# Kernel tuning notes

Measured on AMD Instinct MI355X. Metric: run time of the kernel, lower is better.

The kernel has to match this reference:

```python
import jax, jax.numpy as jnp
import numpy as np

B, S, D = 4, 2048, 1024


def setup_inputs() -> dict:
    key = jax.random.key(0)
    ks = jax.random.split(key, 11)
    sc = 0.02
    f32 = jnp.float32
    return {
        "x1": jax.random.normal(ks[0], (B, S, D), f32),
        "x2": jax.random.normal(ks[1], (B, S, D), f32),
        "x3": jax.random.normal(ks[2], (B, S, D), f32),
        # Stacked per-modality projection weights, stored (in, out) so y = x @ W + b
        "Wq": jax.random.normal(ks[3], (3, D, D), f32) * sc,
        "bq": jax.random.normal(ks[4], (3, D), f32) * sc,
        "Wk": jax.random.normal(ks[5], (3, D, D), f32) * sc,
        "bk": jax.random.normal(ks[6], (3, D), f32) * sc,
        "Wv": jax.random.normal(ks[7], (3, D, D), f32) * sc,
        "bv": jax.random.normal(ks[8], (3, D), f32) * sc,
        "Wo": jax.random.normal(ks[9], (3, 2 * D, D), f32) * sc,
        "bo": jax.random.normal(ks[10], (3, D), f32) * sc,
    }


def reference(x1, x2, x3, Wq, bq, Wk, bk, Wv, bv, Wo, bo):
    x = jnp.stack([x1, x2, x3])                      # (3, B, S, D)
    q = jnp.einsum('mbsd,mde->mbse', x, Wq) + bq[:, None, None, :]
    k = jnp.einsum('mbsd,mde->mbse', x, Wk) + bk[:, None, None, :]
    v = jnp.einsum('mbsd,mde->mbse', x, Wv) + bv[:, None, None, :]
    scale = 1.0 / jnp.sqrt(jnp.asarray(x.shape[-1], x.dtype))
    # self-scores per modality: q_i @ k_i^T
    scores = jnp.einsum('mbsd,mbtd->mbst', q, k) * scale   # (3, B, S, S)
    attn = jax.nn.softmax(scores, axis=-1)
    # context_i = attn_i @ v_{(i+1) mod 3}  (1->2, 2->3, 3->1); dropout is eval-mode identity
    v_next = jnp.roll(v, shift=-1, axis=0)
    ctx = jnp.einsum('mbst,mbtd->mbsd', attn, v_next)      # (3, B, S, D)
    comb = jnp.concatenate([x, ctx], axis=-1)              # (3, B, S, 2D)
    out = jnp.einsum('mbsf,mfd->mbsd', comb, Wo) + bo[:, None, None, :]
    global_feature = jnp.concatenate([out[0], out[1], out[2]], axis=1)  # (B, 3S, D)
    return out[0], out[1], out[2], global_feature
```

## Files before the change

kernel.cpp:

```cpp
#include <hip/hip_runtime.h>
#include <hip/hip_bf16.h>

typedef __bf16 bf16_t;
typedef __bf16 bf16x8 __attribute__((ext_vector_type(8)));
typedef float f32x4 __attribute__((ext_vector_type(4)));

typedef __attribute__((address_space(1))) unsigned int as1_uint;
typedef __attribute__((address_space(3))) unsigned int as3_uint;

#define Bsz 4
#define Ssz 2048
#define Dsz 1024
#define BSD (Bsz * Ssz * Dsz)
#define SCALE_ 0.03125f

__device__ __forceinline__ void gll16(const void* g, void* l) {
  __builtin_amdgcn_global_load_lds((const as1_uint*)g, (as3_uint*)l, 16, 0, 0);
}

__device__ __forceinline__ unsigned bfbits(float f) {
  union { bf16_t h; unsigned short u; } c;
  c.h = (bf16_t)f;
  return (unsigned)c.u;
}

__device__ __forceinline__ void gemm_core(char* AsB, char* BsB,
                                          const bf16_t* A, const bf16_t* A2, int ksplit,
                                          int lda, int lda2,
                                          const bf16_t* Bt, int ldb,
                                          int ktiles, f32x4 acc[4][4]) {
  const int tid = threadIdx.x;
  const int wave = tid >> 6, lane = tid & 63;
  const int quad = lane >> 4, m16 = lane & 15, x7 = lane & 7;
  const int waveM = (wave >> 1) << 6, waveN = (wave & 1) << 6;
  const int srow = tid >> 3;
  const int schunk = (tid & 7) ^ ((tid >> 3) & 7);
  const int ldsbase = wave << 10;

  for (int kt = 0; kt < ktiles; ++kt) {
    const bf16_t* Ak = (kt < ksplit) ? (A + kt * 64) : (A2 + (kt - ksplit) * 64);
    const int ldak = (kt < ksplit) ? lda : lda2;
    const bf16_t* Bk = Bt + kt * 64;
    __syncthreads();
#pragma unroll
    for (int it = 0; it < 4; ++it)
      gll16(Ak + (size_t)(it * 32 + srow) * ldak + schunk * 8, AsB + it * 4096 + ldsbase);
#pragma unroll
    for (int it = 0; it < 4; ++it)
      gll16(Bk + (size_t)(it * 32 + srow) * ldb + schunk * 8, BsB + it * 4096 + ldsbase);
    __syncthreads();
#pragma unroll
    for (int t = 0; t < 2; ++t) {
      bf16x8 a[4], b[4];
      const int cc = t * 4 + quad;
#pragma unroll
      for (int i = 0; i < 4; ++i) {
        const int rr = waveM + i * 16 + m16;
        a[i] = *(const bf16x8*)(AsB + rr * 128 + ((cc ^ x7) << 4));
      }
#pragma unroll
      for (int j = 0; j < 4; ++j) {
        const int rr = waveN + j * 16 + m16;
        b[j] = *(const bf16x8*)(BsB + rr * 128 + ((cc ^ x7) << 4));
      }
#pragma unroll
      for (int i = 0; i < 4; ++i)
#pragma unroll
        for (int j = 0; j < 4; ++j)
          acc[i][j] = __builtin_amdgcn_mfma_f32_16x16x32_bf16(b[j], a[i], acc[i][j], 0, 0, 0);
    }
  }
}

__device__ __forceinline__ ushort4 pack4(const f32x4 v, const float4 b) {
  ushort4 u;
  u.x = (unsigned short)bfbits(v[0] + b.x);
  u.y = (unsigned short)bfbits(v[1] + b.y);
  u.z = (unsigned short)bfbits(v[2] + b.z);
  u.w = (unsigned short)bfbits(v[3] + b.w);
  return u;
}

__global__ __launch_bounds__(256, 2)
void gemm_bt_bf16(const bf16_t* __restrict__ A, long long sAz, int lda,
                  const bf16_t* __restrict__ Bt, long long sBz, int ldb,
                  bf16_t* __restrict__ C, long long sCz, int ldc,
                  int K, int rollB) {
  __shared__ __attribute__((aligned(16))) char smem[32768];
  const int z = blockIdx.z;
  int zb = z;
  if (rollB) { const int m = z >> 2, b = z & 3; zb = ((m + 1) % 3) * Bsz + b; }
  const bf16_t* Az = A + (long long)z * sAz + (size_t)blockIdx.y * 128 * lda;
  const bf16_t* Bz = Bt + (long long)zb * sBz + (size_t)blockIdx.x * 128 * ldb;
  f32x4 acc[4][4];
  const f32x4 zero = {0.f, 0.f, 0.f, 0.f};
#pragma unroll
  for (int i = 0; i < 4; ++i)
#pragma unroll
    for (int j = 0; j < 4; ++j) acc[i][j] = zero;

  gemm_core(smem, smem + 16384, Az, Az, 1 << 30, lda, lda, Bz, ldb, K / 64, acc);

  const int lane = threadIdx.x & 63, wave = threadIdx.x >> 6;
  const int Mb = blockIdx.y * 128 + ((wave >> 1) << 6) + (lane & 15);
  const int Nb = blockIdx.x * 128 + ((wave & 1) << 6) + ((lane >> 4) << 2);
  bf16_t* Cz = C + (long long)z * sCz;
  const float4 zb4 = {0.f, 0.f, 0.f, 0.f};
#pragma unroll
  for (int i = 0; i < 4; ++i) {
    const int M = Mb + i * 16;
#pragma unroll
    for (int j = 0; j < 4; ++j) {
      const int N = Nb + j * 16;
      *(ushort4*)(Cz + (size_t)M * ldc + N) = pack4(acc[i][j], zb4);
    }
  }
}

__global__ __launch_bounds__(256, 2)
void gemm_qkv(const bf16_t* __restrict__ xb, const bf16_t* __restrict__ Wqkvt,
              const float* __restrict__ bq, const float* __restrict__ bk,
              const float* __restrict__ bvp,
              bf16_t* __restrict__ Q, bf16_t* __restrict__ Kb, bf16_t* __restrict__ Vt) {
  __shared__ __attribute__((aligned(16))) char smem[34048];
  const int m = blockIdx.z;
  const int x = blockIdx.x;
  const int which = x >> 3;
  const bf16_t* Az = xb + (size_t)m * BSD + (size_t)blockIdx.y * 128 * Dsz;
  const bf16_t* Bz = Wqkvt + (size_t)m * 3145728 + (size_t)x * 131072;
  f32x4 acc[4][4];
  const f32x4 zero = {0.f, 0.f, 0.f, 0.f};
#pragma unroll
  for (int i = 0; i < 4; ++i)
#pragma unroll
    for (int j = 0; j < 4; ++j) acc[i][j] = zero;

  gemm_core(smem, smem + 16384, Az, Az, 1 << 30, Dsz, Dsz, Bz, Dsz, 16, acc);

  const int tid = threadIdx.x;
  const int lane = tid & 63, wave = tid >> 6;
  const int Ml = ((wave >> 1) << 6) + (lane & 15);
  const int Nl = ((wave & 1) << 6) + ((lane >> 4) << 2);
  const int dseg0 = (x & 7) * 128;
  const float* bb = (which == 0 ? bq : which == 1 ? bk : bvp) + m * Dsz;

  if (which < 2) {
    bf16_t* Cz = (which == 0 ? Q : Kb) + (size_t)m * BSD;
#pragma unroll
    for (int j = 0; j < 4; ++j) {
      const int N = Nl + j * 16;
      const float4 b4 = *(const float4*)(bb + dseg0 + N);
#pragma unroll
      for (int i = 0; i < 4; ++i) {
        const int M = blockIdx.y * 128 + Ml + i * 16;
        *(ushort4*)(Cz + (size_t)M * Dsz + dseg0 + N) = pack4(acc[i][j], b4);
      }
    }
  } else {
    unsigned short* T = (unsigned short*)smem;
    __syncthreads();
#pragma unroll
    for (int j = 0; j < 4; ++j) {
      const int N = Nl + j * 16;
      const float4 b4 = *(const float4*)(bb + dseg0 + N);
      const float bia[4] = {b4.x, b4.y, b4.z, b4.w};
#pragma unroll
      for (int i = 0; i < 4; ++i) {
        const int M = Ml + i * 16;
#pragma unroll
        for (int r = 0; r < 4; ++r)
          T[(N + r) * 132 + M] = (unsigned short)bfbits(acc[i][j][r] + bia[r]);
      }
    }
    __syncthreads();
    const int b = blockIdx.y >> 4;
    const int s0 = (blockIdx.y & 15) * 128;
    bf16_t* Vz = Vt + ((size_t)(m * 4 + b) * 1024 + dseg0) * Ssz;
#pragma unroll
    for (int e = 0; e < 16; ++e) {
      const int idx = e * 256 + tid;
      const int nl = idx >> 5, mc = (idx & 31) * 4;
      const ushort4 u = *(const ushort4*)(T + nl * 132 + mc);
      *(ushort4*)(Vz + (size_t)nl * Ssz + s0 + mc) = u;
    }
  }
}

__global__ __launch_bounds__(256, 2)
void gemm_out(const bf16_t* __restrict__ xb, const bf16_t* __restrict__ ctx,
              const bf16_t* __restrict__ Wot, const float* __restrict__ bo,
              float* __restrict__ out) {
  __shared__ __attribute__((aligned(16))) char smem[32768];
  const int m = blockIdx.z;
  const bf16_t* Az = xb + (size_t)m * BSD + (size_t)blockIdx.y * 128 * Dsz;
  const bf16_t* A2z = ctx + (size_t)m * BSD + (size_t)blockIdx.y * 128 * Dsz;
  const bf16_t* Bz = Wot + (size_t)m * (Dsz * 2 * Dsz) + (size_t)blockIdx.x * 128 * (2 * Dsz);
  f32x4 acc[4][4];
  const f32x4 zero = {0.f, 0.f, 0.f, 0.f};
#pragma unroll
  for (int i = 0; i < 4; ++i)
#pragma unroll
    for (int j = 0; j < 4; ++j) acc[i][j] = zero;

  gemm_core(smem, smem + 16384, Az, A2z, 16, Dsz, Dsz, Bz, 2 * Dsz, 32, acc);

  const int lane = threadIdx.x & 63, wave = threadIdx.x >> 6;
  const int Mb = blockIdx.y * 128 + ((wave >> 1) << 6) + (lane & 15);
  const int Nb = blockIdx.x * 128 + ((wave & 1) << 6) + ((lane >> 4) << 2);
  const float* bz = bo + m * Dsz;
#pragma unroll
  for (int i = 0; i < 4; ++i) {
    const int M = Mb + i * 16;
    const int b = M >> 11, s = M & 2047;
    float* o1 = out + (size_t)m * BSD + (size_t)M * Dsz;
    float* o2 = out + (size_t)3 * BSD + (size_t)b * (3 * Ssz * Dsz) + (size_t)(m * Ssz + s) * Dsz;
#pragma unroll
    for (int j = 0; j < 4; ++j) {
      const int N = Nb + j * 16;
      const float4 b4 = *(const float4*)(bz + N);
      float4 o;
      o.x = acc[i][j][0] + b4.x; o.y = acc[i][j][1] + b4.y;
      o.z = acc[i][j][2] + b4.z; o.w = acc[i][j][3] + b4.w;
      *(float4*)(o1 + N) = o;
      *(float4*)(o2 + N) = o;
    }
  }
}

__global__ __launch_bounds__(256)
void cvt_x(const float* __restrict__ x1, const float* __restrict__ x2,
           const float* __restrict__ x3, bf16_t* __restrict__ xb) {
  const size_t i = ((size_t)blockIdx.x * 256 + threadIdx.x) * 4;
  const float* src;
  size_t off;
  if (i < (size_t)BSD)          { src = x1; off = i; }
  else if (i < (size_t)2 * BSD) { src = x2; off = i - BSD; }
  else                          { src = x3; off = i - (size_t)2 * BSD; }
  const float4 v = *(const float4*)(src + off);
  union { bf16_t h[4]; uint2 u; } o;
  o.h[0] = (bf16_t)v.x; o.h[1] = (bf16_t)v.y; o.h[2] = (bf16_t)v.z; o.h[3] = (bf16_t)v.w;
  *(uint2*)(xb + i) = o.u;
}

__global__ __launch_bounds__(256)
void transpose_to_bf16(const float* __restrict__ in, bf16_t* __restrict__ out,
                       int ldin, int ldout, long long sIn, long long sOut) {
  __shared__ bf16_t Ts[64][65];
  const int t = threadIdx.x;
  const long long z = blockIdx.z;
  const float* inz = in + z * sIn;
  bf16_t* outz = out + z * sOut;
  const int r0 = blockIdx.y << 6, c0 = blockIdx.x << 6;
#pragma unroll
  for (int e = 0; e < 4; ++e) {
    const int idx = (e * 256 + t) * 4;
    const int rr = idx >> 6, cc = idx & 63;
    const float4 v = *(const float4*)(inz + (size_t)(r0 + rr) * ldin + (c0 + cc));
    Ts[rr][cc] = (bf16_t)v.x; Ts[rr][cc + 1] = (bf16_t)v.y;
    Ts[rr][cc + 2] = (bf16_t)v.z; Ts[rr][cc + 3] = (bf16_t)v.w;
  }
  __syncthreads();
#pragma unroll
  for (int e = 0; e < 4; ++e) {
    const int idx = (e * 256 + t) * 4;
    const int oc = idx >> 6, orr = idx & 63;
    union { bf16_t h[4]; uint2 u; } o4;
    o4.h[0] = Ts[orr][oc]; o4.h[1] = Ts[orr + 1][oc];
    o4.h[2] = Ts[orr + 2][oc]; o4.h[3] = Ts[orr + 3][oc];
    *(uint2*)(outz + (size_t)(c0 + oc) * ldout + (r0 + orr)) = o4.u;
  }
}

__global__ __launch_bounds__(256)
void softmax_rows(bf16_t* __restrict__ Sc) {
  const size_t row = blockIdx.x;
  uint4* p = (uint4*)(Sc + row * Ssz);
  const int t = threadIdx.x;
  const int lane = t & 63, wave = t >> 6;
  uint4 u = p[t];
  float v[8];
  v[0] = __uint_as_float(u.x << 16); v[1] = __uint_as_float(u.x & 0xffff0000u);
  v[2] = __uint_as_float(u.y << 16); v[3] = __uint_as_float(u.y & 0xffff0000u);
  v[4] = __uint_as_float(u.z << 16); v[5] = __uint_as_float(u.z & 0xffff0000u);
  v[6] = __uint_as_float(u.w << 16); v[7] = __uint_as_float(u.w & 0xffff0000u);

  float mx = v[0];
#pragma unroll
  for (int i = 1; i < 8; ++i) mx = fmaxf(mx, v[i]);
  for (int o = 32; o > 0; o >>= 1) mx = fmaxf(mx, __shfl_xor(mx, o));
  __shared__ float redm[4], reds[4];
  if (lane == 0) redm[wave] = mx;
  __syncthreads();
  mx = fmaxf(fmaxf(redm[0], redm[1]), fmaxf(redm[2], redm[3]));

  float s = 0.f;
#pragma unroll
  for (int i = 0; i < 8; ++i) { v[i] = __expf((v[i] - mx) * SCALE_); s += v[i]; }
  for (int o = 32; o > 0; o >>= 1) s += __shfl_xor(s, o);
  if (lane == 0) reds[wave] = s;
  __syncthreads();
  s = reds[0] + reds[1] + reds[2] + reds[3];
  const float inv = 1.0f / s;
#pragma unroll
  for (int i = 0; i < 8; ++i) v[i] *= inv;

  u.x = bfbits(v[0]) | (bfbits(v[1]) << 16);
  u.y = bfbits(v[2]) | (bfbits(v[3]) << 16);
  u.z = bfbits(v[4]) | (bfbits(v[5]) << 16);
  u.w = bfbits(v[6]) | (bfbits(v[7]) << 16);
  p[t] = u;
}

extern "C" void kernel_launch(void* const* d_in, const int* in_sizes, int n_in,
                              void* d_out, int out_size, void* d_ws, size_t ws_size,
                              hipStream_t stream) {
  const float* x1 = (const float*)d_in[0];
  const float* x2 = (const float*)d_in[1];
  const float* x3 = (const float*)d_in[2];
  const float* Wq = (const float*)d_in[3];
  const float* bq = (const float*)d_in[4];
  const float* Wk = (const float*)d_in[5];
  const float* bk = (const float*)d_in[6];
  const float* Wv = (const float*)d_in[7];
  const float* bv = (const float*)d_in[8];
  const float* Wo = (const float*)d_in[9];
  const float* bo = (const float*)d_in[10];

  char* ws = (char*)d_ws;
  bf16_t* xb    = (bf16_t*)(ws + 0);
  bf16_t* Wqkvt = (bf16_t*)(ws + 50331648);
  bf16_t* Wot   = (bf16_t*)(ws + 69206016);
  bf16_t* Q     = (bf16_t*)(ws + 81788928);
  bf16_t* Kb    = (bf16_t*)(ws + 132120576);
  bf16_t* Vt    = (bf16_t*)(ws + 182452224);
  bf16_t* Sc    = (bf16_t*)d_out;
  bf16_t* ctx   = Q;

  cvt_x<<<24576, 256, 0, stream>>>(x1, x2, x3, xb);
  transpose_to_bf16<<<dim3(16, 16, 3), 256, 0, stream>>>(Wq, Wqkvt + 0,       1024, 1024, 1048576LL, 3145728LL);
  transpose_to_bf16<<<dim3(16, 16, 3), 256, 0, stream>>>(Wk, Wqkvt + 1048576, 1024, 1024, 1048576LL, 3145728LL);
  transpose_to_bf16<<<dim3(16, 16, 3), 256, 0, stream>>>(Wv, Wqkvt + 2097152, 1024, 1024, 1048576LL, 3145728LL);
  transpose_to_bf16<<<dim3(16, 32, 3), 256, 0, stream>>>(Wo, Wot, 1024, 2048, 2097152LL, 2097152LL);
  gemm_qkv<<<dim3(24, 64, 3), 256, 0, stream>>>(xb, Wqkvt, bq, bk, bv, Q, Kb, Vt);
  gemm_bt_bf16<<<dim3(16, 16, 12), 256, 0, stream>>>(Q, 2097152LL, Dsz, Kb, 2097152LL, Dsz, Sc, 4194304LL, Ssz, Dsz, 0);
  softmax_rows<<<24576, 256, 0, stream>>>(Sc);
  gemm_bt_bf16<<<dim3(8, 16, 12), 256, 0, stream>>>(Sc, 4194304LL, Ssz, Vt, 2097152LL, Ssz, ctx, 2097152LL, Dsz, Ssz, 1);
  gemm_out<<<dim3(8, 64, 3), 256, 0, stream>>>(xb, ctx, Wot, bo, (float*)d_out);
}
```

Measured before the change: 901.1 us.

## Replace GEMM core with 256x256 double-buffered, phase-interleaved 8-wave pipeline

Replaces the 128x128 single-buffered GEMM core with a 256x256 tile, 512-thread core. It double-buffers K tiles in 128KB of LDS, issues global-to-LDS loads for tile t+2 interleaved with MFMA phases, and raises MFMA priority with setprio. All four GEMM kernels, their epilogues (including the V transpose, now done in two halves) and the launch grids are updated to match. The aim is to hide load latency and improve data reuse per byte loaded. The cost is much higher LDS and register pressure per block, so occupancy will be lower, and the grids are smaller.

```diff
diff --git a/kernel.cpp b/kernel.cpp
--- a/kernel.cpp
+++ b/kernel.cpp
@@ -22,54 +22,6 @@
   union { bf16_t h; unsigned short u; } c;
   c.h = (bf16_t)f;
   return (unsigned)c.u;
-}
-
-__device__ __forceinline__ void gemm_core(char* AsB, char* BsB,
-                                          const bf16_t* A, const bf16_t* A2, int ksplit,
-                                          int lda, int lda2,
-                                          const bf16_t* Bt, int ldb,
-                                          int ktiles, f32x4 acc[4][4]) {
-  const int tid = threadIdx.x;
-  const int wave = tid >> 6, lane = tid & 63;
-  const int quad = lane >> 4, m16 = lane & 15, x7 = lane & 7;
-  const int waveM = (wave >> 1) << 6, waveN = (wave & 1) << 6;
-  const int srow = tid >> 3;
-  const int schunk = (tid & 7) ^ ((tid >> 3) & 7);
-  const int ldsbase = wave << 10;
-
-  for (int kt = 0; kt < ktiles; ++kt) {
-    const bf16_t* Ak = (kt < ksplit) ? (A + kt * 64) : (A2 + (kt - ksplit) * 64);
-    const int ldak = (kt < ksplit) ? lda : lda2;
-    const bf16_t* Bk = Bt + kt * 64;
-    __syncthreads();
-#pragma unroll
-    for (int it = 0; it < 4; ++it)
-      gll16(Ak + (size_t)(it * 32 + srow) * ldak + schunk * 8, AsB + it * 4096 + ldsbase);
-#pragma unroll
-    for (int it = 0; it < 4; ++it)
-      gll16(Bk + (size_t)(it * 32 + srow) * ldb + schunk * 8, BsB + it * 4096 + ldsbase);
-    __syncthreads();
-#pragma unroll
-    for (int t = 0; t < 2; ++t) {
-      bf16x8 a[4], b[4];
-      const int cc = t * 4 + quad;
-#pragma unroll
-      for (int i = 0; i < 4; ++i) {
-        const int rr = waveM + i * 16 + m16;
-        a[i] = *(const bf16x8*)(AsB + rr * 128 + ((cc ^ x7) << 4));
-      }
-#pragma unroll
-      for (int j = 0; j < 4; ++j) {
-        const int rr = waveN + j * 16 + m16;
-        b[j] = *(const bf16x8*)(BsB + rr * 128 + ((cc ^ x7) << 4));
-      }
-#pragma unroll
-      for (int i = 0; i < 4; ++i)
-#pragma unroll
-        for (int j = 0; j < 4; ++j)
-          acc[i][j] = __builtin_amdgcn_mfma_f32_16x16x32_bf16(b[j], a[i], acc[i][j], 0, 0, 0);
-    }
-  }
 }
 
 __device__ __forceinline__ ushort4 pack4(const f32x4 v, const float4 b) {
@@ -81,146 +33,272 @@
   return u;
 }
 
-__global__ __launch_bounds__(256, 2)
+__device__ __forceinline__ void mf8(f32x4 acc[8][4], int ib, int jb,
+                                    const bf16x8 b[2], const bf16x8 a[4]) {
+  __builtin_amdgcn_s_setprio(1);
+#pragma unroll
+  for (int i = 0; i < 4; ++i)
+#pragma unroll
+    for (int j = 0; j < 2; ++j)
+      acc[ib + i][jb + j] = __builtin_amdgcn_mfma_f32_16x16x32_bf16(
+          b[j], a[i], acc[ib + i][jb + j], 0, 0, 0);
+  __builtin_amdgcn_s_setprio(0);
+}
+
+#define PHASE_BAR() do {                                   \
+    asm volatile("s_waitcnt lgkmcnt(0)" ::: "memory");     \
+    __builtin_amdgcn_sched_barrier(0);                     \
+    __builtin_amdgcn_s_barrier();                          \
+    __builtin_amdgcn_sched_barrier(0);                     \
+  } while (0)
+
+__device__ __forceinline__ void gemm_core256(char* smem,
+    const bf16_t* A, const bf16_t* A2, int ks, int lda,
+    const bf16_t* Bt, int ldb, int KT, f32x4 acc[8][4]) {
+  const int tid = threadIdx.x;
+  const int wave = tid >> 6, lane = tid & 63;
+  const int quad = lane >> 4, m16 = lane & 15;
+  const int wm = wave >> 2, wn = wave & 3;
+  const int swz = ((quad ^ ((m16 >> 1) & 3)) << 4);
+  const int Ab = ((wm * 128 + m16) << 6) + swz;
+  const int Bb = 32768 + ((wn * 64 + m16) << 6) + swz;
+
+  const int srow = tid >> 2;
+  const int sg = (((tid & 3) ^ ((srow >> 1) & 3)) << 3);
+  const size_t aoff = (size_t)srow * lda + sg;
+  const size_t boff = (size_t)srow * ldb + sg;
+  const size_t astep = (size_t)128 * lda;
+  const size_t bstep = (size_t)128 * ldb;
+  char* ldsW = smem + (wave << 10);
+
+  auto stageA = [&](const bf16_t* As, int sb, int kh) {
+    const bf16_t* s = As + aoff + kh * 32;
+    char* d = ldsW + sb + kh * 16384;
+    gll16(s, d);
+    gll16(s + astep, d + 8192);
+  };
+  auto stageB = [&](const bf16_t* Bs, int sb, int kh) {
+    const bf16_t* s = Bs + boff + kh * 32;
+    char* d = ldsW + sb + 32768 + kh * 16384;
+    gll16(s, d);
+    gll16(s + bstep, d + 8192);
+  };
+
+#pragma unroll
+  for (int t0 = 0; t0 < 2; ++t0) {
+    const bf16_t* As = (t0 < ks) ? (A + t0 * 64) : (A2 + (t0 - ks) * 64);
+    const bf16_t* Bs = Bt + t0 * 64;
+    const int sb = t0 << 16;
+    stageB(Bs, sb, 0); stageB(Bs, sb, 1);
+    stageA(As, sb, 0); stageA(As, sb, 1);
+  }
+
+  bf16x8 a0[4], a1[4], b00[2], b01[2], b10[2], b11[2];
+
+#pragma unroll 1
+  for (int t = 0; t < KT; ++t) {
+    const int cur = (t & 1) << 16;
+    const int tp = (t + 2 < KT) ? (t + 2) : (KT - 1);
+    const bf16_t* As = (tp < ks) ? (A + tp * 64) : (A2 + (tp - ks) * 64);
+    const bf16_t* Bs = Bt + tp * 64;
+    const char* sbp = smem + cur;
+
+    asm volatile("s_waitcnt vmcnt(8)" ::: "memory");
+    __builtin_amdgcn_sched_barrier(0);
+    __builtin_amdgcn_s_barrier();
+    __builtin_amdgcn_sched_barrier(0);
+
+#pragma unroll
+    for (int i = 0; i < 4; ++i) a0[i] = *(const bf16x8*)(sbp + (Ab + i * 1024));
+#pragma unroll
+    for (int j = 0; j < 2; ++j) b00[j] = *(const bf16x8*)(sbp + (Bb + j * 1024));
+    mf8(acc, 0, 0, b00, a0);
+
+#pragma unroll
+    for (int i = 0; i < 4; ++i) a1[i] = *(const bf16x8*)(sbp + (16384 + Ab + i * 1024));
+#pragma unroll
+    for (int j = 0; j < 2; ++j) b01[j] = *(const bf16x8*)(sbp + (16384 + Bb + j * 1024));
+    mf8(acc, 0, 0, b01, a1);
+
+#pragma unroll
+    for (int j = 0; j < 2; ++j) b10[j] = *(const bf16x8*)(sbp + (Bb + 2048 + j * 1024));
+    mf8(acc, 0, 2, b10, a0);
+    PHASE_BAR();
+
+    stageB(Bs, cur, 0);
+#pragma unroll
+    for (int j = 0; j < 2; ++j) b11[j] = *(const bf16x8*)(sbp + (16384 + Bb + 2048 + j * 1024));
+    mf8(acc, 0, 2, b11, a1);
+    PHASE_BAR();
+
+    stageB(Bs, cur, 1);
+#pragma unroll
+    for (int i = 0; i < 4; ++i) a0[i] = *(const bf16x8*)(sbp + (Ab + 4096 + i * 1024));
+    mf8(acc, 4, 0, b00, a0);
+    PHASE_BAR();
+
+    stageA(As, cur, 0);
+#pragma unroll
+    for (int i = 0; i < 4; ++i) a1[i] = *(const bf16x8*)(sbp + (16384 + Ab + 4096 + i * 1024));
+    mf8(acc, 4, 0, b01, a1);
+    PHASE_BAR();
+
+    stageA(As, cur, 1);
+    mf8(acc, 4, 2, b10, a0);
+
+    mf8(acc, 4, 2, b11, a1);
+  }
+
+  asm volatile("s_waitcnt vmcnt(0)" ::: "memory");
+  __builtin_amdgcn_sched_barrier(0);
+}
+
+#define EPI_VARS                                               \
+  const int tid = threadIdx.x, lane = tid & 63, wave = tid >> 6; \
+  const int quad = lane >> 4, m16 = lane & 15;                 \
+  const int wm = wave >> 2, wn = wave & 3;                     \
+  (void)tid; (void)quad; (void)m16; (void)wm; (void)wn;
+#define MLOC(ip) (wm * 128 + (((ip) >> 2) << 6) + (((ip) & 3) << 4) + m16)
+#define NLOC(jp) (wn * 64 + (((jp) >> 1) << 5) + (((jp) & 1) << 4) + (quad << 2))
+
+__global__ __launch_bounds__(512, 2)
 void gemm_bt_bf16(const bf16_t* __restrict__ A, long long sAz, int lda,
                   const bf16_t* __restrict__ Bt, long long sBz, int ldb,
                   bf16_t* __restrict__ C, long long sCz, int ldc,
                   int K, int rollB) {
-  __shared__ __attribute__((aligned(16))) char smem[32768];
+  __shared__ __attribute__((aligned(16))) char smem[131072];
   const int z = blockIdx.z;
   int zb = z;
   if (rollB) { const int m = z >> 2, b = z & 3; zb = ((m + 1) % 3) * Bsz + b; }
-  const bf16_t* Az = A + (long long)z * sAz + (size_t)blockIdx.y * 128 * lda;
-  const bf16_t* Bz = Bt + (long long)zb * sBz + (size_t)blockIdx.x * 128 * ldb;
-  f32x4 acc[4][4];
+  const bf16_t* Az = A + (long long)z * sAz + (size_t)blockIdx.y * 256 * lda;
+  const bf16_t* Bz = Bt + (long long)zb * sBz + (size_t)blockIdx.x * 256 * ldb;
+  f32x4 acc[8][4];
   const f32x4 zero = {0.f, 0.f, 0.f, 0.f};
 #pragma unroll
-  for (int i = 0; i < 4; ++i)
+  for (int i = 0; i < 8; ++i)
 #pragma unroll
     for (int j = 0; j < 4; ++j) acc[i][j] = zero;
 
-  gemm_core(smem, smem + 16384, Az, Az, 1 << 30, lda, lda, Bz, ldb, K / 64, acc);
-
-  const int lane = threadIdx.x & 63, wave = threadIdx.x >> 6;
-  const int Mb = blockIdx.y * 128 + ((wave >> 1) << 6) + (lane & 15);
-  const int Nb = blockIdx.x * 128 + ((wave & 1) << 6) + ((lane >> 4) << 2);
+  gemm_core256(smem, Az, Az, 1 << 30, lda, Bz, ldb, K / 64, acc);
+
+  EPI_VARS;
   bf16_t* Cz = C + (long long)z * sCz;
   const float4 zb4 = {0.f, 0.f, 0.f, 0.f};
 #pragma unroll
-  for (int i = 0; i < 4; ++i) {
-    const int M = Mb + i * 16;
-#pragma unroll
-    for (int j = 0; j < 4; ++j) {
-      const int N = Nb + j * 16;
-      *(ushort4*)(Cz + (size_t)M * ldc + N) = pack4(acc[i][j], zb4);
+  for (int ip = 0; ip < 8; ++ip) {
+    const size_t M = (size_t)blockIdx.y * 256 + MLOC(ip);
+#pragma unroll
+    for (int jp = 0; jp < 4; ++jp) {
+      const int N = blockIdx.x * 256 + NLOC(jp);
+      *(ushort4*)(Cz + M * ldc + N) = pack4(acc[ip][jp], zb4);
     }
   }
 }
 
-__global__ __launch_bounds__(256, 2)
+__global__ __launch_bounds__(512, 2)
 void gemm_qkv(const bf16_t* __restrict__ xb, const bf16_t* __restrict__ Wqkvt,
               const float* __restrict__ bq, const float* __restrict__ bk,
               const float* __restrict__ bvp,
               bf16_t* __restrict__ Q, bf16_t* __restrict__ Kb, bf16_t* __restrict__ Vt) {
-  __shared__ __attribute__((aligned(16))) char smem[34048];
+  __shared__ __attribute__((aligned(16))) char smem[131072];
   const int m = blockIdx.z;
   const int x = blockIdx.x;
-  const int which = x >> 3;
-  const bf16_t* Az = xb + (size_t)m * BSD + (size_t)blockIdx.y * 128 * Dsz;
-  const bf16_t* Bz = Wqkvt + (size_t)m * 3145728 + (size_t)x * 131072;
-  f32x4 acc[4][4];
+  const int which = x >> 2;
+  const bf16_t* Az = xb + (size_t)m * BSD + (size_t)blockIdx.y * 256 * Dsz;
+  const bf16_t* Bz = Wqkvt + (size_t)m * 3145728 + (size_t)x * 262144;
+  f32x4 acc[8][4];
   const f32x4 zero = {0.f, 0.f, 0.f, 0.f};
 #pragma unroll
-  for (int i = 0; i < 4; ++i)
+  for (int i = 0; i < 8; ++i)
 #pragma unroll
     for (int j = 0; j < 4; ++j) acc[i][j] = zero;
 
-  gemm_core(smem, smem + 16384, Az, Az, 1 << 30, Dsz, Dsz, Bz, Dsz, 16, acc);
-
-  const int tid = threadIdx.x;
-  const int lane = tid & 63, wave = tid >> 6;
-  const int Ml = ((wave >> 1) << 6) + (lane & 15);
-  const int Nl = ((wave & 1) << 6) + ((lane >> 4) << 2);
-  const int dseg0 = (x & 7) * 128;
+  gemm_core256(smem, Az, Az, 1 << 30, Dsz, Bz, Dsz, 16, acc);
+
+  EPI_VARS;
+  const int dseg0 = (x & 3) * 256;
   const float* bb = (which == 0 ? bq : which == 1 ? bk : bvp) + m * Dsz;
 
   if (which < 2) {
     bf16_t* Cz = (which == 0 ? Q : Kb) + (size_t)m * BSD;
 #pragma unroll
-    for (int j = 0; j < 4; ++j) {
-      const int N = Nl + j * 16;
+    for (int jp = 0; jp < 4; ++jp) {
+      const int N = NLOC(jp);
       const float4 b4 = *(const float4*)(bb + dseg0 + N);
 #pragma unroll
-      for (int i = 0; i < 4; ++i) {
-        const int M = blockIdx.y * 128 + Ml + i * 16;
-        *(ushort4*)(Cz + (size_t)M * Dsz + dseg0 + N) = pack4(acc[i][j], b4);
+      for (int ip = 0; ip < 8; ++ip) {
+        const size_t M = (size_t)blockIdx.y * 256 + MLOC(ip);
+        *(ushort4*)(Cz + M * Dsz + dseg0 + N) = pack4(acc[ip][jp], b4);
       }
     }
   } else {
     unsigned short* T = (unsigned short*)smem;
-    __syncthreads();
-#pragma unroll
-    for (int j = 0; j < 4; ++j) {
-      const int N = Nl + j * 16;
-      const float4 b4 = *(const float4*)(bb + dseg0 + N);
-      const float bia[4] = {b4.x, b4.y, b4.z, b4.w};
-#pragma unroll
-      for (int i = 0; i < 4; ++i) {
-        const int M = Ml + i * 16;
-#pragma unroll
-        for (int r = 0; r < 4; ++r)
-          T[(N + r) * 132 + M] = (unsigned short)bfbits(acc[i][j][r] + bia[r]);
+    const int b = blockIdx.y >> 3;
+    const int s0 = (blockIdx.y & 7) * 256;
+    bf16_t* Vz = Vt + ((size_t)(m * 4 + b) * 1024 + dseg0) * (size_t)Ssz;
+#pragma unroll
+    for (int nh = 0; nh < 2; ++nh) {
+      __syncthreads();
+      if ((wn >> 1) == nh) {
+#pragma unroll
+        for (int jp = 0; jp < 4; ++jp) {
+          const int Nh = ((wn & 1) << 6) + (((jp) >> 1) << 5) + (((jp) & 1) << 4) + (quad << 2);
+          const float4 b4 = *(const float4*)(bb + dseg0 + nh * 128 + Nh);
+          const float bia[4] = {b4.x, b4.y, b4.z, b4.w};
+#pragma unroll
+          for (int ip = 0; ip < 8; ++ip) {
+            const int M = MLOC(ip);
+#pragma unroll
+            for (int r = 0; r < 4; ++r)
+              T[(Nh + r) * 264 + M] = (unsigned short)bfbits(acc[ip][jp][r] + bia[r]);
+          }
+        }
+      }
+      __syncthreads();
+#pragma unroll
+      for (int e = 0; e < 8; ++e) {
+        const int c = e * 512 + tid;
+        const int n = c >> 5, mc = (c & 31) * 8;
+        *(uint4*)(Vz + (size_t)(nh * 128 + n) * Ssz + s0 + mc) =
+            *(const uint4*)(T + n * 264 + mc);
       }
     }
-    __syncthreads();
-    const int b = blockIdx.y >> 4;
-    const int s0 = (blockIdx.y & 15) * 128;
-    bf16_t* Vz = Vt + ((size_t)(m * 4 + b) * 1024 + dseg0) * Ssz;
-#pragma unroll
-    for (int e = 0; e < 16; ++e) {
-      const int idx = e * 256 + tid;
-      const int nl = idx >> 5, mc = (idx & 31) * 4;
-      const ushort4 u = *(const ushort4*)(T + nl * 132 + mc);
-      *(ushort4*)(Vz + (size_t)nl * Ssz + s0 + mc) = u;
-    }
-  }
-}
-
-__global__ __launch_bounds__(256, 2)
+  }
+}
+
+__global__ __launch_bounds__(512, 2)
 void gemm_out(const bf16_t* __restrict__ xb, const bf16_t* __restrict__ ctx,
               const bf16_t* __restrict__ Wot, const float* __restrict__ bo,
               float* __restrict__ out) {
-  __shared__ __attribute__((aligned(16))) char smem[32768];
+  __shared__ __attribute__((aligned(16))) char smem[131072];
   const int m = blockIdx.z;
-  const bf16_t* Az = xb + (size_t)m * BSD + (size_t)blockIdx.y * 128 * Dsz;
-  const bf16_t* A2z = ctx + (size_t)m * BSD + (size_t)blockIdx.y * 128 * Dsz;
-  const bf16_t* Bz = Wot + (size_t)m * (Dsz * 2 * Dsz) + (size_t)blockIdx.x * 128 * (2 * Dsz);
-  f32x4 acc[4][4];
+  const bf16_t* Az = xb + (size_t)m * BSD + (size_t)blockIdx.y * 256 * Dsz;
+  const bf16_t* A2z = ctx + (size_t)m * BSD + (size_t)blockIdx.y * 256 * Dsz;
+  const bf16_t* Bz = Wot + (size_t)m * (Dsz * 2 * Dsz) + (size_t)blockIdx.x * 256 * (2 * Dsz);
+  f32x4 acc[8][4];
   const f32x4 zero = {0.f, 0.f, 0.f, 0.f};
 #pragma unroll
-  for (int i = 0; i < 4; ++i)
+  for (int i = 0; i < 8; ++i)
 #pragma unroll
     for (int j = 0; j < 4; ++j) acc[i][j] = zero;
 
-  gemm_core(smem, smem + 16384, Az, A2z, 16, Dsz, Dsz, Bz, 2 * Dsz, 32, acc);
-
-  const int lane = threadIdx.x & 63, wave = threadIdx.x >> 6;
-  const int Mb = blockIdx.y * 128 + ((wave >> 1) << 6) + (lane & 15);
-  const int Nb = blockIdx.x * 128 + ((wave & 1) << 6) + ((lane >> 4) << 2);
+  gemm_core256(smem, Az, A2z, 16, Dsz, Bz, 2 * Dsz, 32, acc);
+
+  EPI_VARS;
   const float* bz = bo + m * Dsz;
 #pragma unroll
-  for (int i = 0; i < 4; ++i) {
-    const int M = Mb + i * 16;
+  for (int ip = 0; ip < 8; ++ip) {
+    const int M = blockIdx.y * 256 + MLOC(ip);
     const int b = M >> 11, s = M & 2047;
     float* o1 = out + (size_t)m * BSD + (size_t)M * Dsz;
     float* o2 = out + (size_t)3 * BSD + (size_t)b * (3 * Ssz * Dsz) + (size_t)(m * Ssz + s) * Dsz;
 #pragma unroll
-    for (int j = 0; j < 4; ++j) {
-      const int N = Nb + j * 16;
+    for (int jp = 0; jp < 4; ++jp) {
+      const int N = blockIdx.x * 256 + NLOC(jp);
       const float4 b4 = *(const float4*)(bz + N);
       float4 o;
-      o.x = acc[i][j][0] + b4.x; o.y = acc[i][j][1] + b4.y;
-      o.z = acc[i][j][2] + b4.z; o.w = acc[i][j][3] + b4.w;
+      o.x = acc[ip][jp][0] + b4.x; o.y = acc[ip][jp][1] + b4.y;
+      o.z = acc[ip][jp][2] + b4.z; o.w = acc[ip][jp][3] + b4.w;
       *(float4*)(o1 + N) = o;
       *(float4*)(o2 + N) = o;
     }
@@ -341,9 +419,9 @@
   transpose_to_bf16<<<dim3(16, 16, 3), 256, 0, stream>>>(Wk, Wqkvt + 1048576, 1024, 1024, 1048576LL, 3145728LL);
   transpose_to_bf16<<<dim3(16, 16, 3), 256, 0, stream>>>(Wv, Wqkvt + 2097152, 1024, 1024, 1048576LL, 3145728LL);
   transpose_to_bf16<<<dim3(16, 32, 3), 256, 0, stream>>>(Wo, Wot, 1024, 2048, 2097152LL, 2097152LL);
-  gemm_qkv<<<dim3(24, 64, 3), 256, 0, stream>>>(xb, Wqkvt, bq, bk, bv, Q, Kb, Vt);
-  gemm_bt_bf16<<<dim3(16, 16, 12), 256, 0, stream>>>(Q, 2097152LL, Dsz, Kb, 2097152LL, Dsz, Sc, 4194304LL, Ssz, Dsz, 0);
+  gemm_qkv<<<dim3(12, 32, 3), 512, 0, stream>>>(xb, Wqkvt, bq, bk, bv, Q, Kb, Vt);
+  gemm_bt_bf16<<<dim3(8, 8, 12), 512, 0, stream>>>(Q, 2097152LL, Dsz, Kb, 2097152LL, Dsz, Sc, 4194304LL, Ssz, Dsz, 0);
   softmax_rows<<<24576, 256, 0, stream>>>(Sc);
-  gemm_bt_bf16<<<dim3(8, 16, 12), 256, 0, stream>>>(Sc, 4194304LL, Ssz, Vt, 2097152LL, Ssz, ctx, 2097152LL, Dsz, Ssz, 1);
-  gemm_out<<<dim3(8, 64, 3), 256, 0, stream>>>(xb, ctx, Wot, bo, (float*)d_out);
-}
+  gemm_bt_bf16<<<dim3(4, 8, 12), 512, 0, stream>>>(Sc, 4194304LL, Ssz, Vt, 2097152LL, Ssz, ctx, 2097152LL, Dsz, Ssz, 1);
+  gemm_out<<<dim3(4, 32, 3), 512, 0, stream>>>(xb, ctx, Wot, bo, (float*)d_out);
+}
```

Measured after the change: 921.9 us. 2.3% more time.

## Swizzle GEMM block indices across XCDs and raise launch-bounds occupancy to 4

Applied to the files above, without the earlier changes.

Adds an XCD-aware block index remap so that consecutive blocks dispatched round-robin to the 8 XCDs cover contiguous row bands, which improves L2 reuse of A and B tiles within each XCD. It also raises the launch-bounds minimum blocks per CU from 2 to 4 on the three GEMM kernels, which caps register use so more blocks can be resident. The tighter register budget risks spills in the 4x4 accumulator MFMA loop. The remap also assumes the grid Y dimension is divisible by 8.

```diff
diff --git a/kernel.cpp b/kernel.cpp
--- a/kernel.cpp
+++ b/kernel.cpp
@@ -22,6 +22,14 @@
   union { bf16_t h; unsigned short u; } c;
   c.h = (bf16_t)f;
   return (unsigned)c.u;
+}
+
+__device__ __forceinline__ void xcd_swz(int bx, int by, int GX, int GY,
+                                        int* nx, int* ny) {
+  const int L = bx + GX * by;
+  const int xcd = L & 7, idx = L >> 3;
+  *nx = idx % GX;
+  *ny = (GY >> 3) * xcd + idx / GX;
 }
 
 __device__ __forceinline__ void gemm_core(char* AsB, char* BsB,
@@ -81,7 +89,7 @@
   return u;
 }
 
-__global__ __launch_bounds__(256, 2)
+__global__ __launch_bounds__(256, 4)
 void gemm_bt_bf16(const bf16_t* __restrict__ A, long long sAz, int lda,
                   const bf16_t* __restrict__ Bt, long long sBz, int ldb,
                   bf16_t* __restrict__ C, long long sCz, int ldc,
@@ -90,8 +98,10 @@
   const int z = blockIdx.z;
   int zb = z;
   if (rollB) { const int m = z >> 2, b = z & 3; zb = ((m + 1) % 3) * Bsz + b; }
-  const bf16_t* Az = A + (long long)z * sAz + (size_t)blockIdx.y * 128 * lda;
-  const bf16_t* Bz = Bt + (long long)zb * sBz + (size_t)blockIdx.x * 128 * ldb;
+  int nx, ny;
+  xcd_swz(blockIdx.x, blockIdx.y, gridDim.x, gridDim.y, &nx, &ny);
+  const bf16_t* Az = A + (long long)z * sAz + (size_t)ny * 128 * lda;
+  const bf16_t* Bz = Bt + (long long)zb * sBz + (size_t)nx * 128 * ldb;
   f32x4 acc[4][4];
   const f32x4 zero = {0.f, 0.f, 0.f, 0.f};
 #pragma unroll
@@ -102,8 +112,8 @@
   gemm_core(smem, smem + 16384, Az, Az, 1 << 30, lda, lda, Bz, ldb, K / 64, acc);
 
   const int lane = threadIdx.x & 63, wave = threadIdx.x >> 6;
-  const int Mb = blockIdx.y * 128 + ((wave >> 1) << 6) + (lane & 15);
-  const int Nb = blockIdx.x * 128 + ((wave & 1) << 6) + ((lane >> 4) << 2);
+  const int Mb = ny * 128 + ((wave >> 1) << 6) + (lane & 15);
+  const int Nb = nx * 128 + ((wave & 1) << 6) + ((lane >> 4) << 2);
   bf16_t* Cz = C + (long long)z * sCz;
   const float4 zb4 = {0.f, 0.f, 0.f, 0.f};
 #pragma unroll
@@ -117,16 +127,17 @@
   }
 }
 
-__global__ __launch_bounds__(256, 2)
+__global__ __launch_bounds__(256, 4)
 void gemm_qkv(const bf16_t* __restrict__ xb, const bf16_t* __restrict__ Wqkvt,
               const float* __restrict__ bq, const float* __restrict__ bk,
               const float* __restrict__ bvp,
               bf16_t* __restrict__ Q, bf16_t* __restrict__ Kb, bf16_t* __restrict__ Vt) {
   __shared__ __attribute__((aligned(16))) char smem[34048];
   const int m = blockIdx.z;
-  const int x = blockIdx.x;
+  int x, by;
+  xcd_swz(blockIdx.x, blockIdx.y, 24, 64, &x, &by);
   const int which = x >> 3;
-  const bf16_t* Az = xb + (size_t)m * BSD + (size_t)blockIdx.y * 128 * Dsz;
+  const bf16_t* Az = xb + (size_t)m * BSD + (size_t)by * 128 * Dsz;
   const bf16_t* Bz = Wqkvt + (size_t)m * 3145728 + (size_t)x * 131072;
   f32x4 acc[4][4];
   const f32x4 zero = {0.f, 0.f, 0.f, 0.f};
@@ -152,7 +163,7 @@
       const float4 b4 = *(const float4*)(bb + dseg0 + N);
 #pragma unroll
       for (int i = 0; i < 4; ++i) {
-        const int M = blockIdx.y * 128 + Ml + i * 16;
+        const int M = by * 128 + Ml + i * 16;
         *(ushort4*)(Cz + (size_t)M * Dsz + dseg0 + N) = pack4(acc[i][j], b4);
       }
     }
@@ -173,8 +184,8 @@
       }
     }
     __syncthreads();
-    const int b = blockIdx.y >> 4;
-    const int s0 = (blockIdx.y & 15) * 128;
+    const int b = by >> 4;
+    const int s0 = (by & 15) * 128;
     bf16_t* Vz = Vt + ((size_t)(m * 4 + b) * 1024 + dseg0) * Ssz;
 #pragma unroll
     for (int e = 0; e < 16; ++e) {
@@ -186,15 +197,17 @@
   }
 }
 
-__global__ __launch_bounds__(256, 2)
+__global__ __launch_bounds__(256, 4)
 void gemm_out(const bf16_t* __restrict__ xb, const bf16_t* __restrict__ ctx,
               const bf16_t* __restrict__ Wot, const float* __restrict__ bo,
               float* __restrict__ out) {
   __shared__ __attribute__((aligned(16))) char smem[32768];
   const int m = blockIdx.z;
-  const bf16_t* Az = xb + (size_t)m * BSD + (size_t)blockIdx.y * 128 * Dsz;
-  const bf16_t* A2z = ctx + (size_t)m * BSD + (size_t)blockIdx.y * 128 * Dsz;
-  const bf16_t* Bz = Wot + (size_t)m * (Dsz * 2 * Dsz) + (size_t)blockIdx.x * 128 * (2 * Dsz);
+  int nx, ny;
+  xcd_swz(blockIdx.x, blockIdx.y, 8, 64, &nx, &ny);
+  const bf16_t* Az = xb + (size_t)m * BSD + (size_t)ny * 128 * Dsz;
+  const bf16_t* A2z = ctx + (size_t)m * BSD + (size_t)ny * 128 * Dsz;
+  const bf16_t* Bz = Wot + (size_t)m * (Dsz * 2 * Dsz) + (size_t)nx * 128 * (2 * Dsz);
   f32x4 acc[4][4];
   const f32x4 zero = {0.f, 0.f, 0.f, 0.f};
 #pragma unroll
@@ -205,8 +218,8 @@
   gemm_core(smem, smem + 16384, Az, A2z, 16, Dsz, Dsz, Bz, 2 * Dsz, 32, acc);
 
   const int lane = threadIdx.x & 63, wave = threadIdx.x >> 6;
-  const int Mb = blockIdx.y * 128 + ((wave >> 1) << 6) + (lane & 15);
-  const int Nb = blockIdx.x * 128 + ((wave & 1) << 6) + ((lane >> 4) << 2);
+  const int Mb = ny * 128 + ((wave >> 1) << 6) + (lane & 15);
+  const int Nb = nx * 128 + ((wave & 1) << 6) + ((lane >> 4) << 2);
   const float* bz = bo + m * Dsz;
 #pragma unroll
   for (int i = 0; i < 4; ++i) {
```

Result: faster. 877.2 us (-2.6%).
